# Performance work log

Measured on AMD Instinct MI355X. Metric: run time of the kernel, lower is better.

The kernel has to match this reference:

```python
import jax, jax.numpy as jnp
import numpy as np

B, N, C = 4, 1370, 1024
H = 16
DH = C // H
HID = 4 * C
EPS = 1e-5
LS_INIT = 1e-5


def layernorm(x, g, b):
    mu = jnp.mean(x, axis=-1, keepdims=True)
    var = jnp.var(x, axis=-1, keepdims=True)
    return (x - mu) * jax.lax.rsqrt(var + EPS) * g + b


def setup_inputs() -> dict:
    key = jax.random.key(0)
    ks = jax.random.split(key, 16)
    s = lambda k, shp, scale: jax.random.normal(k, shp, dtype=jnp.float32) * scale
    return {
        "x": s(ks[0], (B, N, C), 1.0),
        "ln1_g": jnp.ones((C,), jnp.float32),
        "ln1_b": jnp.zeros((C,), jnp.float32),
        "w_qkv": s(ks[1], (3 * C, C), 0.02),
        "b_qkv": jnp.zeros((3 * C,), jnp.float32),
        "w_proj": s(ks[2], (C, C), 0.02),
        "b_proj": jnp.zeros((C,), jnp.float32),
        "gamma1": jnp.full((C,), LS_INIT, jnp.float32),
        "ln2_g": jnp.ones((C,), jnp.float32),
        "ln2_b": jnp.zeros((C,), jnp.float32),
        "w_fc1": s(ks[3], (HID, C), 0.02),
        "b_fc1": jnp.zeros((HID,), jnp.float32),
        "w_fc2": s(ks[4], (C, HID), 0.02),
        "b_fc2": jnp.zeros((C,), jnp.float32),
        "gamma2": jnp.full((C,), LS_INIT, jnp.float32),
    }


def block_forward(x, ln1_g, ln1_b, w_qkv, b_qkv, w_proj, b_proj, gamma1,
                  ln2_g, ln2_b, w_fc1, b_fc1, w_fc2, b_fc2, gamma2):
    # attention residual branch
    h = layernorm(x, ln1_g, ln1_b)
    qkv = h @ w_qkv.T + b_qkv                      # [B,N,3C]
    qkv = qkv.reshape(B, N, 3, H, DH).transpose(2, 0, 3, 1, 4)  # [3,B,H,N,DH]
    q, k, v = qkv[0] * (DH ** -0.5), qkv[1], qkv[2]
    attn = jax.nn.softmax(jnp.einsum('bhnd,bhmd->bhnm', q, k), axis=-1)
    o = jnp.einsum('bhnm,bhmd->bhnd', attn, v)     # [B,H,N,DH]
    o = o.transpose(0, 2, 1, 3).reshape(B, N, C)
    o = o @ w_proj.T + b_proj
    x = x + o * gamma1
    # MLP residual branch
    h = layernorm(x, ln2_g, ln2_b)
    h = jax.nn.gelu(h @ w_fc1.T + b_fc1, approximate=False)
    h = h @ w_fc2.T + b_fc2
    return x + h * gamma2


def reference(x, ln1_g, ln1_b, w_qkv, b_qkv, w_proj, b_proj, gamma1,
              ln2_g, ln2_b, w_fc1, b_fc1, w_fc2, b_fc2, gamma2):
    return block_forward(x, ln1_g, ln1_b, w_qkv, b_qkv, w_proj, b_proj, gamma1,
                         ln2_g, ln2_b, w_fc1, b_fc1, w_fc2, b_fc2, gamma2)
```

## Files before the change

kernel.cpp:

```cpp
#include <hip/hip_runtime.h>
#include <hip/hip_bf16.h>
#include <math.h>

#define B_ 4
#define N_ 1370
#define C_ 1024
#define H_ 16
#define DH_ 64
#define HID_ 4096
#define M_ (B_*N_)
#define MPAD 5504
#define NKV 1408

typedef short v8s __attribute__((ext_vector_type(8)));
typedef short v4s16 __attribute__((ext_vector_type(4)));
typedef float v4f __attribute__((ext_vector_type(4)));
typedef float v16f __attribute__((ext_vector_type(16)));
typedef int v4i __attribute__((ext_vector_type(4)));
typedef int v8i __attribute__((ext_vector_type(8)));

__device__ __forceinline__ short f2bf(float x) {
  union { float f; unsigned u; } a; a.f = x;
  unsigned r = (a.u + 0x7fffu + ((a.u >> 16) & 1u)) >> 16;
  return (short)r;
}

__device__ __forceinline__ void gl_lds16(const void* g, void* l) {
  __builtin_amdgcn_global_load_lds(
      (const __attribute__((address_space(1))) unsigned int*)g,
      (__attribute__((address_space(3))) unsigned int*)l, 16, 0, 0);
}

__global__ __launch_bounds__(256) void cast_w(const float* __restrict__ wq, const float* __restrict__ wp,
                                              const float* __restrict__ w1, const float* __restrict__ w2,
                                              char* __restrict__ w8) {
  int i = blockIdx.x * 256 + threadIdx.x;
  int e = i << 2;
  const float* src; int off;
  if (e < 3145728)      { src = wq; off = e; }
  else if (e < 4194304) { src = wp; off = e - 3145728; }
  else if (e < 8388608) { src = w1; off = e - 4194304; }
  else                  { src = w2; off = e - 8388608; }
  float4 v = *reinterpret_cast<const float4*>(src + off);
  int pk = __builtin_amdgcn_cvt_pk_fp8_f32(v.x, v.y, 0, false);
  pk = __builtin_amdgcn_cvt_pk_fp8_f32(v.z, v.w, pk, true);
  *reinterpret_cast<int*>(w8 + e) = pk;
}

__global__ __launch_bounds__(256) void ln8_k(const float* __restrict__ x, const float* __restrict__ g,
                                             const float* __restrict__ bt, char* __restrict__ out, int mreal) {
  int row = blockIdx.x, t = threadIdx.x;
  char* orow = out + (size_t)row * C_;
  if (row >= mreal) {
    *reinterpret_cast<int*>(orow + (t << 2)) = 0;
    return;
  }
  float4 v = reinterpret_cast<const float4*>(x + (size_t)row * C_)[t];
  float s = v.x + v.y + v.z + v.w;
  float q = v.x*v.x + v.y*v.y + v.z*v.z + v.w*v.w;
#pragma unroll
  for (int m = 1; m < 64; m <<= 1) { s += __shfl_xor(s, m); q += __shfl_xor(q, m); }
  __shared__ float sb[8];
  int w = t >> 6;
  if ((t & 63) == 0) { sb[w] = s; sb[4 + w] = q; }
  __syncthreads();
  s = sb[0] + sb[1] + sb[2] + sb[3];
  q = sb[4] + sb[5] + sb[6] + sb[7];
  float mean = s * (1.f / C_);
  float rstd = rsqrtf(q * (1.f / C_) - mean * mean + 1e-5f);
  float4 gv = reinterpret_cast<const float4*>(g)[t];
  float4 bv = reinterpret_cast<const float4*>(bt)[t];
  float o0 = (v.x - mean) * rstd * gv.x + bv.x;
  float o1 = (v.y - mean) * rstd * gv.y + bv.y;
  float o2 = (v.z - mean) * rstd * gv.z + bv.z;
  float o3 = (v.w - mean) * rstd * gv.w + bv.w;
  int pk = __builtin_amdgcn_cvt_pk_fp8_f32(o0, o1, 0, false);
  pk = __builtin_amdgcn_cvt_pk_fp8_f32(o2, o3, pk, true);
  *reinterpret_cast<int*>(orow + (t << 2)) = pk;
}

template<int MODE8, int BM8>
__global__ __launch_bounds__(256) void gemm8_k(
    const char* __restrict__ A, const char* __restrict__ Bw,
    const float* __restrict__ bias, const float* __restrict__ resid,
    const float* __restrict__ gamma, char* __restrict__ o8,
    short* __restrict__ obf, float* __restrict__ of32,
    int K, int Nc, int mreal, int nTm)
{
  constexpr int MF8 = BM8 / 64;
  __shared__ char As[3][BM8 * 64];
  __shared__ char Bs[3][128 * 64];
  int tid = threadIdx.x;
  int lane = tid & 63, wave = tid >> 6;
  int l31 = lane & 31, hi = lane >> 5;
  int nwg = gridDim.x;
  int sidx = blockIdx.x;
  int ord = (sidx & 7) * (nwg >> 3) + (sidx >> 3);
  int tn = ord / nTm, tm = ord % nTm;
  int wr = wave >> 1, wc = wave & 1;

  v16f acc[MF8][2];
#pragma unroll
  for (int m = 0; m < MF8; m++)
#pragma unroll
    for (int n = 0; n < 2; n++)
#pragma unroll
      for (int r = 0; r < 16; r++) acc[m][n][r] = 0.f;

  int srow = wave * 16 + (lane >> 2);
  int sch = ((lane & 3) ^ ((srow >> 1) & 3)) << 4;
  const char* Ag = A + (size_t)(tm * BM8 + srow) * K + sch;
  const char* Bg = Bw + (size_t)(tn * 128 + srow) * K + sch;

#define STAGE8(bi, k0)                                                   \
  do {                                                                   \
    gl_lds16(Ag + (k0), &As[bi][wave * 1024]);                           \
    if constexpr (BM8 == 128)                                            \
      gl_lds16(Ag + (size_t)64 * K + (k0), &As[bi][4096 + wave * 1024]); \
    gl_lds16(Bg + (k0), &Bs[bi][wave * 1024]);                           \
    gl_lds16(Bg + (size_t)64 * K + (k0), &Bs[bi][4096 + wave * 1024]);   \
  } while (0)

  int kT = K >> 6;

  STAGE8(0, 0);
  STAGE8(1, 64);
  STAGE8(2, 128);

  int rowA = wr * (BM8 / 2) + l31;
  int rowB = wc * 64 + l31;
  int swA = (rowA >> 1) & 3, swB = (rowB >> 1) & 3;

  auto body = [&](int t, int bb, bool stage_next) {
    __builtin_amdgcn_s_barrier();
    union { v4i q[2]; v8i v; } fa[MF8], fb[2];
#pragma unroll
    for (int m = 0; m < MF8; m++) {
      int row = rowA + m * 32;
      fa[m].q[0] = *reinterpret_cast<const v4i*>(&As[bb][row * 64 + (((2 * hi + 0) ^ swA) << 4)]);
      fa[m].q[1] = *reinterpret_cast<const v4i*>(&As[bb][row * 64 + (((2 * hi + 1) ^ swA) << 4)]);
    }
#pragma unroll
    for (int n = 0; n < 2; n++) {
      int row = rowB + n * 32;
      fb[n].q[0] = *reinterpret_cast<const v4i*>(&Bs[bb][row * 64 + (((2 * hi + 0) ^ swB) << 4)]);
      fb[n].q[1] = *reinterpret_cast<const v4i*>(&Bs[bb][row * 64 + (((2 * hi + 1) ^ swB) << 4)]);
    }
    asm volatile("s_waitcnt lgkmcnt(0)" ::: "memory");
    __builtin_amdgcn_s_barrier();
    if (stage_next) STAGE8(bb, (size_t)(t + 3) << 6);
    __builtin_amdgcn_s_setprio(1);
#pragma unroll
    for (int m = 0; m < MF8; m++)
#pragma unroll
      for (int n = 0; n < 2; n++)
        acc[m][n] = __builtin_amdgcn_mfma_scale_f32_32x32x64_f8f6f4(
            fa[m].v, fb[n].v, acc[m][n], 0, 0, 0, 0x7f7f7f7f, 0, 0x7f7f7f7f);
    __builtin_amdgcn_s_setprio(0);
  };

  int b = 0, t = 0;
  for (; t < kT - 2; ++t) {
    if constexpr (BM8 == 128) asm volatile("s_waitcnt vmcnt(8)" ::: "memory");
    else                      asm volatile("s_waitcnt vmcnt(6)" ::: "memory");
    body(t, b, t + 3 < kT);
    b = (b == 2) ? 0 : b + 1;
  }
  if constexpr (BM8 == 128) asm volatile("s_waitcnt vmcnt(4)" ::: "memory");
  else                      asm volatile("s_waitcnt vmcnt(3)" ::: "memory");
  body(kT - 2, b, false);
  b = (b == 2) ? 0 : b + 1;
  asm volatile("s_waitcnt vmcnt(0)" ::: "memory");
  body(kT - 1, b, false);
#undef STAGE8

#pragma unroll
  for (int m = 0; m < MF8; m++) {
#pragma unroll
    for (int n = 0; n < 2; n++) {
      int gc = tn * 128 + wc * 64 + n * 32 + l31;
      float bb = bias[gc];
      float gm = (MODE8 == 1) ? gamma[gc] : 0.f;
#pragma unroll
      for (int r = 0; r < 16; r++) {
        int crow = (r & 3) + 8 * (r >> 2) + 4 * hi;
        int gr = tm * BM8 + wr * (BM8 / 2) + m * 32 + crow;
        float v = acc[m][n][r] + bb;
        if (MODE8 == 0) {
          float sc = (gc < 1024) ? 0.18033688011112042f : 1.0f;
          obf[(size_t)gr * Nc + gc] = f2bf(v * sc);
        } else if (MODE8 == 2) {
          float gl = 0.5f * v * (1.f + erff(v * 0.70710678f));
          int pk = __builtin_amdgcn_cvt_pk_fp8_f32(gl, gl, 0, false);
          o8[(size_t)gr * Nc + gc] = (char)(pk & 0xff);
        } else {
          if (gr < mreal) of32[(size_t)gr * Nc + gc] = resid[(size_t)gr * Nc + gc] + gm * v;
        }
      }
    }
  }
}

__global__ __launch_bounds__(256) void vtrans_k(const short* __restrict__ qkv, short* __restrict__ vt) {
  int kt = blockIdx.x;
  int bh = blockIdx.y;
  int b = bh >> 4, h = bh & 15;
  int t = threadIdx.x;
  __shared__ short T[128][76];
  int n0 = kt * 128;
  int r = t >> 1;
  int c0 = (t & 1) * 32;
  int tok = n0 + r;
  int tokc = tok < N_ ? tok : N_ - 1;
  const short* src = qkv + (size_t)(b * N_ + tokc) * 3072 + 2048 + h * 64 + c0;
  v8s a0 = *reinterpret_cast<const v8s*>(src);
  v8s a1 = *reinterpret_cast<const v8s*>(src + 8);
  v8s a2 = *reinterpret_cast<const v8s*>(src + 16);
  v8s a3 = *reinterpret_cast<const v8s*>(src + 24);
  *reinterpret_cast<v8s*>(&T[r][c0]) = a0;
  *reinterpret_cast<v8s*>(&T[r][c0 + 8]) = a1;
  *reinterpret_cast<v8s*>(&T[r][c0 + 16]) = a2;
  *reinterpret_cast<v8s*>(&T[r][c0 + 24]) = a3;
  __syncthreads();
  int d = t & 63;
  int k0 = (t >> 6) * 32;
  short tmp[32];
#pragma unroll
  for (int j = 0; j < 32; j++) tmp[j] = T[k0 + j][d];
  short* dst = vt + ((size_t)bh * 64 + d) * NKV + n0 + k0;
#pragma unroll
  for (int j = 0; j < 32; j += 8)
    *reinterpret_cast<v8s*>(dst + j) = *reinterpret_cast<const v8s*>(&tmp[j]);
}

__device__ __forceinline__ v8s pack_swap(const float* p) {
  unsigned w0, w1, w2, w3;
  asm("v_cvt_pk_bf16_f32 %0, %1, %2" : "=v"(w0) : "v"(p[0]), "v"(p[1]));
  asm("v_cvt_pk_bf16_f32 %0, %1, %2" : "=v"(w1) : "v"(p[2]), "v"(p[3]));
  asm("v_cvt_pk_bf16_f32 %0, %1, %2" : "=v"(w2) : "v"(p[4]), "v"(p[5]));
  asm("v_cvt_pk_bf16_f32 %0, %1, %2" : "=v"(w3) : "v"(p[6]), "v"(p[7]));
  asm("v_permlane32_swap_b32 %0, %1" : "+v"(w0), "+v"(w2));
  asm("v_permlane32_swap_b32 %0, %1" : "+v"(w1), "+v"(w3));
  union { unsigned u[4]; v8s s; } r;
  r.u[0] = w0; r.u[1] = w1; r.u[2] = w2; r.u[3] = w3;
  return r.s;
}

__global__ __launch_bounds__(256) void attn_k(const short* __restrict__ qkv, const short* __restrict__ vt,
                                              char* __restrict__ o8)
{
  int s = blockIdx.x + 11 * blockIdx.y;
  int ord = (s & 7) * 88 + (s >> 3);
  int qt = ord % 11, bh = ord / 11;
  int b = bh >> 4, h = bh & 15;
  int tid = threadIdx.x;
  int lane = tid & 63, wave = tid >> 6;
  int l31 = lane & 31, hi = lane >> 5;

  __shared__ short Ks[2][64 * 64];
  __shared__ short Vs[2][64 * 64];

  int qrow = qt * 128 + wave * 32 + l31;
  int qc = qrow < N_ ? qrow : N_ - 1;
  const short* qp = qkv + (size_t)(b * N_ + qc) * 3072 + h * 64;
  v8s qf[4];
#pragma unroll
  for (int i = 0; i < 4; i++) qf[i] = *reinterpret_cast<const v8s*>(qp + i * 16 + hi * 8);

  v16f oa0, oa1;
#pragma unroll
  for (int r = 0; r < 16; r++) { oa0[r] = 0.f; oa1[r] = 0.f; }
  float ls = 0.f;

  int kvA = wave * 8 + (lane >> 3);
  int kchunk = ((lane & 7) ^ (kvA & 7)) << 3;
  int vdA = wave * 16 + (lane >> 3);
  int vdB = vdA + 8;
  const short* kApt = qkv + (size_t)(b * N_ + kvA) * 3072 + 1024 + h * 64 + kchunk;
  const short* kBpt = kApt + (size_t)32 * 3072;
  const short* vbase = vt + (size_t)bh * 64 * NKV;
  const short* vApt = vbase + (size_t)vdA * NKV + (((lane & 7) ^ ((vdA >> 1) & 7)) << 3);
  const short* vBpt = vbase + (size_t)vdB * NKV + (((lane & 7) ^ ((vdB >> 1) & 7)) << 3);

  const int NT = NKV / 64;
  gl_lds16(kApt, &Ks[0][wave * 512]);
  gl_lds16(kBpt, &Ks[0][2048 + wave * 512]);
  gl_lds16(vApt, &Vs[0][wave * 1024]);
  gl_lds16(vBpt, &Vs[0][wave * 1024 + 512]);
  kApt += 64 * 3072; kBpt += 64 * 3072; vApt += 64; vBpt += 64;
  __syncthreads();
  int bi = 0;
  for (int t = 0; t < NT; ++t) {
    int kv0 = t * 64;
    if (t + 1 < NT) {
      gl_lds16(kApt, &Ks[bi ^ 1][wave * 512]);
      gl_lds16(kBpt, &Ks[bi ^ 1][2048 + wave * 512]);
      gl_lds16(vApt, &Vs[bi ^ 1][wave * 1024]);
      gl_lds16(vBpt, &Vs[bi ^ 1][wave * 1024 + 512]);
      kApt += 64 * 3072; kBpt += 64 * 3072; vApt += 64; vBpt += 64;
    }

    v16f s0, s1;
#pragma unroll
    for (int r = 0; r < 16; r++) { s0[r] = 0.f; s1[r] = 0.f; }
#pragma unroll
    for (int i = 0; i < 4; i++) {
      int c0 = ((2 * i + hi) ^ (l31 & 7)) << 3;
      v8s ka = *reinterpret_cast<const v8s*>(&Ks[bi][l31 * 64 + c0]);
      v8s kb = *reinterpret_cast<const v8s*>(&Ks[bi][(32 + l31) * 64 + c0]);
      s0 = __builtin_amdgcn_mfma_f32_32x32x16_bf16(ka, qf[i], s0, 0, 0, 0);
      s1 = __builtin_amdgcn_mfma_f32_32x32x16_bf16(kb, qf[i], s1, 0, 0, 0);
    }

    if (kv0 + 64 > N_) {
#pragma unroll
      for (int r = 0; r < 16; r++) {
        int crow = (r & 3) + 8 * (r >> 2) + 4 * hi;
        if (kv0 + crow >= N_) s0[r] = -1e30f;
        if (kv0 + 32 + crow >= N_) s1[r] = -1e30f;
      }
    }

    float p0[16], p1[16];
#pragma unroll
    for (int r = 0; r < 16; r++) p0[r] = exp2f(s0[r]);
#pragma unroll
    for (int r = 0; r < 16; r++) p1[r] = exp2f(s1[r]);
    float t0[8];
#pragma unroll
    for (int j = 0; j < 8; j++)
      t0[j] = (p0[2 * j] + p0[2 * j + 1]) + (p1[2 * j] + p1[2 * j + 1]);
    float t1[4];
#pragma unroll
    for (int j = 0; j < 4; j++) t1[j] = t0[2 * j] + t0[2 * j + 1];
    float psum = (t1[0] + t1[1]) + (t1[2] + t1[3]);
    psum += __shfl_xor(psum, 32);
    ls += psum;

    v8s pa0 = pack_swap(p0), pa1 = pack_swap(p0 + 8), pa2 = pack_swap(p1), pa3 = pack_swap(p1 + 8);

#pragma unroll
    for (int i = 0; i < 4; i++) {
      v8s pai = (i == 0) ? pa0 : (i == 1) ? pa1 : (i == 2) ? pa2 : pa3;
      int cc = ((2 * i + hi) ^ ((l31 >> 1) & 7)) << 3;
      v8s v0f = *reinterpret_cast<const v8s*>(&Vs[bi][l31 * 64 + cc]);
      v8s v1f = *reinterpret_cast<const v8s*>(&Vs[bi][(32 + l31) * 64 + cc]);
      oa0 = __builtin_amdgcn_mfma_f32_32x32x16_bf16(pai, v0f, oa0, 0, 0, 0);
      oa1 = __builtin_amdgcn_mfma_f32_32x32x16_bf16(pai, v1f, oa1, 0, 0, 0);
    }
    __syncthreads();
    bi ^= 1;
  }

  float inv = 1.f / ls;
#pragma unroll
  for (int r = 0; r < 16; r++) {
    int crow = (r & 3) + 8 * (r >> 2) + 4 * hi;
    float iv = __shfl(inv, crow);
    int qg = qt * 128 + wave * 32 + crow;
    if (qg < N_) {
      size_t base = (size_t)(b * N_ + qg) * 1024 + h * 64;
      float a0 = oa0[r] * iv, a1 = oa1[r] * iv;
      int pk0 = __builtin_amdgcn_cvt_pk_fp8_f32(a0, a0, 0, false);
      int pk1 = __builtin_amdgcn_cvt_pk_fp8_f32(a1, a1, 0, false);
      o8[base + l31] = (char)(pk0 & 0xff);
      o8[base + 32 + l31] = (char)(pk1 & 0xff);
    }
  }
}

extern "C" void kernel_launch(void* const* d_in, const int* in_sizes, int n_in,
                              void* d_out, int out_size, void* d_ws, size_t ws_size,
                              hipStream_t stream) {
  const float* x     = (const float*)d_in[0];
  const float* ln1g  = (const float*)d_in[1];
  const float* ln1b  = (const float*)d_in[2];
  const float* wqkv  = (const float*)d_in[3];
  const float* bqkv  = (const float*)d_in[4];
  const float* wproj = (const float*)d_in[5];
  const float* bproj = (const float*)d_in[6];
  const float* g1    = (const float*)d_in[7];
  const float* ln2g  = (const float*)d_in[8];
  const float* ln2b  = (const float*)d_in[9];
  const float* wfc1  = (const float*)d_in[10];
  const float* bfc1  = (const float*)d_in[11];
  const float* wfc2  = (const float*)d_in[12];
  const float* bfc2  = (const float*)d_in[13];
  const float* g2    = (const float*)d_in[14];
  float* out = (float*)d_out;

  char* p = (char*)d_ws;
  char*  w8    = p;
  char*  h8    = p + 12582912;
  short* qkvb  = (short*)(p + 18219008);
  char*  mlp8  = (char*)(p + 18219008);
  char*  ob8   = p + 52035584;
  float* x2    = (float*)(p + 57671680);
  short* vtg   = (short*)x2;

  cast_w<<<12288, 256, 0, stream>>>(wqkv, wproj, wfc1, wfc2, w8);
  ln8_k<<<MPAD, 256, 0, stream>>>(x, ln1g, ln1b, h8, M_);
  gemm8_k<0, 128><<<1032, 256, 0, stream>>>(h8, w8, bqkv, nullptr, nullptr,
                                            nullptr, qkvb, nullptr, 1024, 3072, M_, 43);
  vtrans_k<<<dim3(11, 64), 256, 0, stream>>>(qkvb, vtg);
  attn_k<<<dim3(11, 64), 256, 0, stream>>>(qkvb, vtg, ob8);
  gemm8_k<1, 64><<<688, 256, 0, stream>>>(ob8, w8 + 3145728, bproj, x, g1,
                                          nullptr, nullptr, x2, 1024, 1024, M_, 86);
  ln8_k<<<MPAD, 256, 0, stream>>>(x2, ln2g, ln2b, h8, M_);
  gemm8_k<2, 128><<<1376, 256, 0, stream>>>(h8, w8 + 4194304, bfc1, nullptr, nullptr,
                                            mlp8, nullptr, nullptr, 1024, 4096, M_, 43);
  gemm8_k<1, 64><<<688, 256, 0, stream>>>(mlp8, w8 + 8388608, bfc2, x2, g2,
                                          nullptr, nullptr, out, 4096, 1024, M_, 86);
}
```

Measured before the change: 258.2 us.

## Switch attention to FP8 MFMA and fuse V transpose into QKV GEMM epilogue

The QKV GEMM epilogue now writes Q, K and a pre-transposed, swizzled V directly in FP8 into separate buffers, which removes the separate V-transpose kernel and halves the intermediate traffic. The attention kernel uses scaled 32x32x64 FP8 MFMAs for both QK^T and PV, with the P matrix packed to FP8, in place of bf16 MFMAs. Load and LDS footprints per tile drop, and a memset of the V buffer is added for padding. The trade-off is lower precision in attention scores and probabilities, plus scattered byte stores in the GEMM epilogue.

Result: slower. 292.8 us (+13.4%).

```diff
diff --git a/kernel.cpp b/kernel.cpp
--- a/kernel.cpp
+++ b/kernel.cpp
@@ -12,17 +12,14 @@
 #define MPAD 5504
 #define NKV 1408
 
-typedef short v8s __attribute__((ext_vector_type(8)));
 typedef short v4s16 __attribute__((ext_vector_type(4)));
-typedef float v4f __attribute__((ext_vector_type(4)));
 typedef float v16f __attribute__((ext_vector_type(16)));
 typedef int v4i __attribute__((ext_vector_type(4)));
 typedef int v8i __attribute__((ext_vector_type(8)));
 
-__device__ __forceinline__ short f2bf(float x) {
-  union { float f; unsigned u; } a; a.f = x;
-  unsigned r = (a.u + 0x7fffu + ((a.u >> 16) & 1u)) >> 16;
-  return (short)r;
+__device__ __forceinline__ char f2fp8(float x) {
+  int pk = __builtin_amdgcn_cvt_pk_fp8_f32(x, x, 0, false);
+  return (char)(pk & 0xff);
 }
 
 __device__ __forceinline__ void gl_lds16(const void* g, void* l) {
@@ -84,7 +81,7 @@
     const char* __restrict__ A, const char* __restrict__ Bw,
     const float* __restrict__ bias, const float* __restrict__ resid,
     const float* __restrict__ gamma, char* __restrict__ o8,
-    short* __restrict__ obf, float* __restrict__ of32,
+    float* __restrict__ of32, char* __restrict__ ok8, char* __restrict__ ov8,
     int K, int Nc, int mreal, int nTm)
 {
   constexpr int MF8 = BM8 / 64;
@@ -187,12 +184,25 @@
         int gr = tm * BM8 + wr * (BM8 / 2) + m * 32 + crow;
         float v = acc[m][n][r] + bb;
         if (MODE8 == 0) {
-          float sc = (gc < 1024) ? 0.18033688011112042f : 1.0f;
-          obf[(size_t)gr * Nc + gc] = f2bf(v * sc);
+          if (gc < 1024) {
+            o8[(size_t)gr * 1024 + gc] = f2fp8(v * 0.18033688011112042f);
+          } else if (gc < 2048) {
+            ok8[(size_t)gr * 1024 + gc - 1024] = f2fp8(v);
+          } else {
+            int dd = gc & 63;
+            int hh = (gc >> 6) & 15;
+            int b2 = (gr >= 1370) + (gr >= 2740) + (gr >= 4110);
+            int n2 = gr - b2 * 1370;
+            int kvin = n2 & 31, blk = (n2 >> 5) & 1;
+            int hi16 = (kvin >> 2) & 1;
+            int rr = (kvin & 3) + ((kvin >> 3) << 2);
+            int cph = hi16 | ((blk ^ ((dd >> 1) & 1)) << 1);
+            int col = (n2 & ~63) + (cph << 4) + rr;
+            ov8[((size_t)((b2 * 16 + hh) * 64 + dd)) * NKV + col] = f2fp8(v);
+          }
         } else if (MODE8 == 2) {
           float gl = 0.5f * v * (1.f + erff(v * 0.70710678f));
-          int pk = __builtin_amdgcn_cvt_pk_fp8_f32(gl, gl, 0, false);
-          o8[(size_t)gr * Nc + gc] = (char)(pk & 0xff);
+          o8[(size_t)gr * Nc + gc] = f2fp8(gl);
         } else {
           if (gr < mreal) of32[(size_t)gr * Nc + gc] = resid[(size_t)gr * Nc + gc] + gm * v;
         }
@@ -201,53 +211,8 @@
   }
 }
 
-__global__ __launch_bounds__(256) void vtrans_k(const short* __restrict__ qkv, short* __restrict__ vt) {
-  int kt = blockIdx.x;
-  int bh = blockIdx.y;
-  int b = bh >> 4, h = bh & 15;
-  int t = threadIdx.x;
-  __shared__ short T[128][76];
-  int n0 = kt * 128;
-  int r = t >> 1;
-  int c0 = (t & 1) * 32;
-  int tok = n0 + r;
-  int tokc = tok < N_ ? tok : N_ - 1;
-  const short* src = qkv + (size_t)(b * N_ + tokc) * 3072 + 2048 + h * 64 + c0;
-  v8s a0 = *reinterpret_cast<const v8s*>(src);
-  v8s a1 = *reinterpret_cast<const v8s*>(src + 8);
-  v8s a2 = *reinterpret_cast<const v8s*>(src + 16);
-  v8s a3 = *reinterpret_cast<const v8s*>(src + 24);
-  *reinterpret_cast<v8s*>(&T[r][c0]) = a0;
-  *reinterpret_cast<v8s*>(&T[r][c0 + 8]) = a1;
-  *reinterpret_cast<v8s*>(&T[r][c0 + 16]) = a2;
-  *reinterpret_cast<v8s*>(&T[r][c0 + 24]) = a3;
-  __syncthreads();
-  int d = t & 63;
-  int k0 = (t >> 6) * 32;
-  short tmp[32];
-#pragma unroll
-  for (int j = 0; j < 32; j++) tmp[j] = T[k0 + j][d];
-  short* dst = vt + ((size_t)bh * 64 + d) * NKV + n0 + k0;
-#pragma unroll
-  for (int j = 0; j < 32; j += 8)
-    *reinterpret_cast<v8s*>(dst + j) = *reinterpret_cast<const v8s*>(&tmp[j]);
-}
-
-__device__ __forceinline__ v8s pack_swap(const float* p) {
-  unsigned w0, w1, w2, w3;
-  asm("v_cvt_pk_bf16_f32 %0, %1, %2" : "=v"(w0) : "v"(p[0]), "v"(p[1]));
-  asm("v_cvt_pk_bf16_f32 %0, %1, %2" : "=v"(w1) : "v"(p[2]), "v"(p[3]));
-  asm("v_cvt_pk_bf16_f32 %0, %1, %2" : "=v"(w2) : "v"(p[4]), "v"(p[5]));
-  asm("v_cvt_pk_bf16_f32 %0, %1, %2" : "=v"(w3) : "v"(p[6]), "v"(p[7]));
-  asm("v_permlane32_swap_b32 %0, %1" : "+v"(w0), "+v"(w2));
-  asm("v_permlane32_swap_b32 %0, %1" : "+v"(w1), "+v"(w3));
-  union { unsigned u[4]; v8s s; } r;
-  r.u[0] = w0; r.u[1] = w1; r.u[2] = w2; r.u[3] = w3;
-  return r.s;
-}
-
-__global__ __launch_bounds__(256) void attn_k(const short* __restrict__ qkv, const short* __restrict__ vt,
-                                              char* __restrict__ o8)
+__global__ __launch_bounds__(256) void attn_k(const char* __restrict__ q8, const char* __restrict__ k8,
+                                              const char* __restrict__ vt8, char* __restrict__ o8)
 {
   int s = blockIdx.x + 11 * blockIdx.y;
   int ord = (s & 7) * 88 + (s >> 3);
@@ -257,60 +222,53 @@
   int lane = tid & 63, wave = tid >> 6;
   int l31 = lane & 31, hi = lane >> 5;
 
-  __shared__ short Ks[2][64 * 64];
-  __shared__ short Vs[2][64 * 64];
+  __shared__ char Ks[2][4096];
+  __shared__ char Vs[2][4096];
+
+  union F8 { v4i q[2]; v8i v; unsigned u[8]; };
 
   int qrow = qt * 128 + wave * 32 + l31;
   int qc = qrow < N_ ? qrow : N_ - 1;
-  const short* qp = qkv + (size_t)(b * N_ + qc) * 3072 + h * 64;
-  v8s qf[4];
-#pragma unroll
-  for (int i = 0; i < 4; i++) qf[i] = *reinterpret_cast<const v8s*>(qp + i * 16 + hi * 8);
+  const char* qp = q8 + (size_t)(b * N_ + qc) * 1024 + h * 64 + hi * 32;
+  F8 qf;
+  qf.q[0] = *reinterpret_cast<const v4i*>(qp);
+  qf.q[1] = *reinterpret_cast<const v4i*>(qp + 16);
 
   v16f oa0, oa1;
 #pragma unroll
   for (int r = 0; r < 16; r++) { oa0[r] = 0.f; oa1[r] = 0.f; }
   float ls = 0.f;
 
-  int kvA = wave * 8 + (lane >> 3);
-  int kchunk = ((lane & 7) ^ (kvA & 7)) << 3;
-  int vdA = wave * 16 + (lane >> 3);
-  int vdB = vdA + 8;
-  const short* kApt = qkv + (size_t)(b * N_ + kvA) * 3072 + 1024 + h * 64 + kchunk;
-  const short* kBpt = kApt + (size_t)32 * 3072;
-  const short* vbase = vt + (size_t)bh * 64 * NKV;
-  const short* vApt = vbase + (size_t)vdA * NKV + (((lane & 7) ^ ((vdA >> 1) & 7)) << 3);
-  const short* vBpt = vbase + (size_t)vdB * NKV + (((lane & 7) ^ ((vdB >> 1) & 7)) << 3);
+  int kvl = tid >> 2;
+  int kc = (((tid & 3) ^ ((kvl >> 1) & 1)) << 4);
+  const char* kpt = k8 + (size_t)(b * N_ + kvl) * 1024 + h * 64 + kc;
+  const char* vpt = vt8 + ((size_t)(bh * 64) + (tid >> 2)) * NKV + ((tid & 3) << 4);
 
   const int NT = NKV / 64;
-  gl_lds16(kApt, &Ks[0][wave * 512]);
-  gl_lds16(kBpt, &Ks[0][2048 + wave * 512]);
-  gl_lds16(vApt, &Vs[0][wave * 1024]);
-  gl_lds16(vBpt, &Vs[0][wave * 1024 + 512]);
-  kApt += 64 * 3072; kBpt += 64 * 3072; vApt += 64; vBpt += 64;
+  gl_lds16(kpt, &Ks[0][wave * 1024]);
+  gl_lds16(vpt, &Vs[0][wave * 1024]);
+  kpt += (size_t)64 * 1024; vpt += 64;
   __syncthreads();
   int bi = 0;
+  int kx = (l31 >> 1) & 1;
   for (int t = 0; t < NT; ++t) {
     int kv0 = t * 64;
     if (t + 1 < NT) {
-      gl_lds16(kApt, &Ks[bi ^ 1][wave * 512]);
-      gl_lds16(kBpt, &Ks[bi ^ 1][2048 + wave * 512]);
-      gl_lds16(vApt, &Vs[bi ^ 1][wave * 1024]);
-      gl_lds16(vBpt, &Vs[bi ^ 1][wave * 1024 + 512]);
-      kApt += 64 * 3072; kBpt += 64 * 3072; vApt += 64; vBpt += 64;
-    }
-
+      gl_lds16(kpt, &Ks[bi ^ 1][wave * 1024]);
+      gl_lds16(vpt, &Vs[bi ^ 1][wave * 1024]);
+      kpt += (size_t)64 * 1024; vpt += 64;
+    }
+
+    F8 ka, kb;
+    ka.q[0] = *reinterpret_cast<const v4i*>(&Ks[bi][l31 * 64 + ((2 * hi + kx) << 4)]);
+    ka.q[1] = *reinterpret_cast<const v4i*>(&Ks[bi][l31 * 64 + ((2 * hi + (1 ^ kx)) << 4)]);
+    kb.q[0] = *reinterpret_cast<const v4i*>(&Ks[bi][(32 + l31) * 64 + ((2 * hi + kx) << 4)]);
+    kb.q[1] = *reinterpret_cast<const v4i*>(&Ks[bi][(32 + l31) * 64 + ((2 * hi + (1 ^ kx)) << 4)]);
     v16f s0, s1;
 #pragma unroll
     for (int r = 0; r < 16; r++) { s0[r] = 0.f; s1[r] = 0.f; }
-#pragma unroll
-    for (int i = 0; i < 4; i++) {
-      int c0 = ((2 * i + hi) ^ (l31 & 7)) << 3;
-      v8s ka = *reinterpret_cast<const v8s*>(&Ks[bi][l31 * 64 + c0]);
-      v8s kb = *reinterpret_cast<const v8s*>(&Ks[bi][(32 + l31) * 64 + c0]);
-      s0 = __builtin_amdgcn_mfma_f32_32x32x16_bf16(ka, qf[i], s0, 0, 0, 0);
-      s1 = __builtin_amdgcn_mfma_f32_32x32x16_bf16(kb, qf[i], s1, 0, 0, 0);
-    }
+    s0 = __builtin_amdgcn_mfma_scale_f32_32x32x64_f8f6f4(ka.v, qf.v, s0, 0, 0, 0, 0x7f7f7f7f, 0, 0x7f7f7f7f);
+    s1 = __builtin_amdgcn_mfma_scale_f32_32x32x64_f8f6f4(kb.v, qf.v, s1, 0, 0, 0, 0x7f7f7f7f, 0, 0x7f7f7f7f);
 
     if (kv0 + 64 > N_) {
 #pragma unroll
@@ -337,17 +295,26 @@
     psum += __shfl_xor(psum, 32);
     ls += psum;
 
-    v8s pa0 = pack_swap(p0), pa1 = pack_swap(p0 + 8), pa2 = pack_swap(p1), pa3 = pack_swap(p1 + 8);
-
-#pragma unroll
-    for (int i = 0; i < 4; i++) {
-      v8s pai = (i == 0) ? pa0 : (i == 1) ? pa1 : (i == 2) ? pa2 : pa3;
-      int cc = ((2 * i + hi) ^ ((l31 >> 1) & 7)) << 3;
-      v8s v0f = *reinterpret_cast<const v8s*>(&Vs[bi][l31 * 64 + cc]);
-      v8s v1f = *reinterpret_cast<const v8s*>(&Vs[bi][(32 + l31) * 64 + cc]);
-      oa0 = __builtin_amdgcn_mfma_f32_32x32x16_bf16(pai, v0f, oa0, 0, 0, 0);
-      oa1 = __builtin_amdgcn_mfma_f32_32x32x16_bf16(pai, v1f, oa1, 0, 0, 0);
-    }
+    F8 pf;
+#pragma unroll
+    for (int w = 0; w < 4; w++) {
+      int pk = __builtin_amdgcn_cvt_pk_fp8_f32(p0[4 * w], p0[4 * w + 1], 0, false);
+      pf.u[w] = (unsigned)__builtin_amdgcn_cvt_pk_fp8_f32(p0[4 * w + 2], p0[4 * w + 3], pk, true);
+    }
+#pragma unroll
+    for (int w = 0; w < 4; w++) {
+      int pk = __builtin_amdgcn_cvt_pk_fp8_f32(p1[4 * w], p1[4 * w + 1], 0, false);
+      pf.u[4 + w] = (unsigned)__builtin_amdgcn_cvt_pk_fp8_f32(p1[4 * w + 2], p1[4 * w + 3], pk, true);
+    }
+
+    F8 va, vb;
+    va.q[0] = *reinterpret_cast<const v4i*>(&Vs[bi][l31 * 64 + ((hi + 2 * kx) << 4)]);
+    va.q[1] = *reinterpret_cast<const v4i*>(&Vs[bi][l31 * 64 + ((hi + 2 * (1 ^ kx)) << 4)]);
+    vb.q[0] = *reinterpret_cast<const v4i*>(&Vs[bi][(32 + l31) * 64 + ((hi + 2 * kx) << 4)]);
+    vb.q[1] = *reinterpret_cast<const v4i*>(&Vs[bi][(32 + l31) * 64 + ((hi + 2 * (1 ^ kx)) << 4)]);
+    oa0 = __builtin_amdgcn_mfma_scale_f32_32x32x64_f8f6f4(pf.v, va.v, oa0, 0, 0, 0, 0x7f7f7f7f, 0, 0x7f7f7f7f);
+    oa1 = __builtin_amdgcn_mfma_scale_f32_32x32x64_f8f6f4(pf.v, vb.v, oa1, 0, 0, 0, 0x7f7f7f7f, 0, 0x7f7f7f7f);
+
     __syncthreads();
     bi ^= 1;
   }
@@ -360,11 +327,8 @@
     int qg = qt * 128 + wave * 32 + crow;
     if (qg < N_) {
       size_t base = (size_t)(b * N_ + qg) * 1024 + h * 64;
-      float a0 = oa0[r] * iv, a1 = oa1[r] * iv;
-      int pk0 = __builtin_amdgcn_cvt_pk_fp8_f32(a0, a0, 0, false);
-      int pk1 = __builtin_amdgcn_cvt_pk_fp8_f32(a1, a1, 0, false);
-      o8[base + l31] = (char)(pk0 & 0xff);
-      o8[base + 32 + l31] = (char)(pk1 & 0xff);
+      o8[base + l31] = f2fp8(oa0[r] * iv);
+      o8[base + 32 + l31] = f2fp8(oa1[r] * iv);
     }
   }
 }
@@ -390,25 +354,26 @@
   float* out = (float*)d_out;
 
   char* p = (char*)d_ws;
-  char*  w8    = p;
-  char*  h8    = p + 12582912;
-  short* qkvb  = (short*)(p + 18219008);
-  char*  mlp8  = (char*)(p + 18219008);
-  char*  ob8   = p + 52035584;
-  float* x2    = (float*)(p + 57671680);
-  short* vtg   = (short*)x2;
-
+  char*  w8   = p;
+  char*  h8   = p + 12582912;
+  char*  q8   = p + 18219008;
+  char*  k8   = p + 23986176;
+  char*  vt8  = p + 29753344;
+  char*  ob8  = p + 35520512;
+  float* x2   = (float*)(p + 41156608);
+  char*  mlp8 = p + 63700992;
+
+  hipMemsetAsync(vt8, 0, 5767168, stream);
   cast_w<<<12288, 256, 0, stream>>>(wqkv, wproj, wfc1, wfc2, w8);
   ln8_k<<<MPAD, 256, 0, stream>>>(x, ln1g, ln1b, h8, M_);
   gemm8_k<0, 128><<<1032, 256, 0, stream>>>(h8, w8, bqkv, nullptr, nullptr,
-                                            nullptr, qkvb, nullptr, 1024, 3072, M_, 43);
-  vtrans_k<<<dim3(11, 64), 256, 0, stream>>>(qkvb, vtg);
-  attn_k<<<dim3(11, 64), 256, 0, stream>>>(qkvb, vtg, ob8);
+                                            q8, nullptr, k8, vt8, 1024, 3072, M_, 43);
+  attn_k<<<dim3(11, 64), 256, 0, stream>>>(q8, k8, vt8, ob8);
   gemm8_k<1, 64><<<688, 256, 0, stream>>>(ob8, w8 + 3145728, bproj, x, g1,
-                                          nullptr, nullptr, x2, 1024, 1024, M_, 86);
+                                          nullptr, x2, nullptr, nullptr, 1024, 1024, M_, 86);
   ln8_k<<<MPAD, 256, 0, stream>>>(x2, ln2g, ln2b, h8, M_);
   gemm8_k<2, 128><<<1376, 256, 0, stream>>>(h8, w8 + 4194304, bfc1, nullptr, nullptr,
-                                            mlp8, nullptr, nullptr, 1024, 4096, M_, 43);
+                                            mlp8, nullptr, nullptr, nullptr, 1024, 4096, M_, 43);
   gemm8_k<1, 64><<<688, 256, 0, stream>>>(mlp8, w8 + 8388608, bfc2, x2, g2,
-                                          nullptr, nullptr, out, 4096, 1024, M_, 86);
-}
+                                          nullptr, out, nullptr, nullptr, 4096, 1024, M_, 86);
+}
```
